# Performance work log

Measured on AMD Instinct MI355X. Metric: run time of the kernel, lower is better.

Reference implementation:

```python
import jax, jax.numpy as jnp
import numpy as np

B, K, T, C = 4, 8, 2048, 64

def setup_inputs() -> dict:
    key = jax.random.key(0)
    ks = jax.random.split(key, 7)
    return {
        "x": jax.random.normal(ks[0], (B, K, T, C), dtype=jnp.float32),
        "Wq": jax.random.normal(ks[1], (C, C), dtype=jnp.float32) / np.sqrt(C),
        "bq": jax.random.normal(ks[2], (C,), dtype=jnp.float32) * 0.01,
        "Wk": jax.random.normal(ks[3], (C, C), dtype=jnp.float32) / np.sqrt(C),
        "bk": jax.random.normal(ks[4], (C,), dtype=jnp.float32) * 0.01,
        "Wv": jax.random.normal(ks[5], (C, C), dtype=jnp.float32) / np.sqrt(C),
        "bv": jax.random.normal(ks[6], (C,), dtype=jnp.float32) * 0.01,
    }

def reference(x, Wq, bq, Wk, bk, Wv, bv):
    c_dim = x.shape[-1]
    # torch nn.Linear: y = x @ W.T + b
    q = jnp.einsum('bktc,dc->bktd', x, Wq) + bq
    k = jnp.einsum('bktc,dc->bktd', x, Wk) + bk
    v = jnp.einsum('bktc,dc->bktd', x, Wv) + bv
    scores = jnp.einsum('bkic,bkjc->bkij', q, k) / jnp.sqrt(jnp.float32(c_dim))
    attn = jax.nn.softmax(scores, axis=-1)
    out = jnp.einsum('bkij,bkjc->bkic', attn, v)
    return out
```

## Files before the change

### kernel.cpp

```cpp
#include <hip/hip_runtime.h>


#define T_DIM 2048
#define NHEAD 32
#define HSTRIDE (T_DIM * 64)
#define QSCALE 0.18033688011112042f
#define SOFF  8.0f

#define SWZ(row, grp) ((row) * 64 + ((((grp) ^ ((row) & 7)) & 7) * 8))

#define RAW_BARRIER() asm volatile("s_waitcnt lgkmcnt(0)\n\ts_barrier" ::: "memory")

typedef _Float16 h8 __attribute__((ext_vector_type(8)));
typedef _Float16 h4 __attribute__((ext_vector_type(4)));
typedef __fp16   g2 __attribute__((ext_vector_type(2)));
typedef float    f4 __attribute__((ext_vector_type(4)));
typedef float    fv16 __attribute__((ext_vector_type(16)));

union H4U { h4 v; g2 p[2]; };
union H8U { h8 v; h4 h[2]; g2 p[4]; };

#if defined(__has_builtin)
#if __has_builtin(__builtin_amdgcn_exp2f)
#define EXP2(x) __builtin_amdgcn_exp2f(x)
#endif
#endif
#ifndef EXP2
__device__ inline float exp2_raw(float x) {
    float r;
    asm("v_exp_f32 %0, %1" : "=v"(r) : "v"(x));
    return r;
}
#define EXP2(x) exp2_raw(x)
#endif

__device__ inline h4 cvt4(f4 x) {
    H4U u;
    u.p[0] = __builtin_amdgcn_cvt_pkrtz(x[0], x[1]);
    u.p[1] = __builtin_amdgcn_cvt_pkrtz(x[2], x[3]);
    return u.v;
}

__device__ inline h8 cvt8(f4 a, f4 b) {
    H8U r;
    r.h[0] = cvt4(a);
    r.h[1] = cvt4(b);
    return r.v;
}

__device__ inline fv16 splat16(float x) {
    fv16 r;
    #pragma unroll
    for (int i = 0; i < 16; ++i) r[i] = x;
    return r;
}

__global__ __launch_bounds__(256) void qkv_proj_kernel(
    const float* __restrict__ x,
    const float* __restrict__ Wq, const float* __restrict__ bq,
    const float* __restrict__ Wk, const float* __restrict__ bk,
    const float* __restrict__ Wv, const float* __restrict__ bv,
    _Float16* __restrict__ qh, _Float16* __restrict__ khT,
    _Float16* __restrict__ vtT)
{
    __shared__ _Float16 ws[3][64 * 64];
    __shared__ float bsh[3][64];

    const int tid  = threadIdx.x;
    const int row0 = blockIdx.x * 64;
    const int head = blockIdx.x >> 5;
    const int t0   = (blockIdx.x & 31) * 64;

    const int w    = tid >> 6;
    const int lane = tid & 63;
    const int l15  = lane & 15;
    const int qd   = lane >> 4;

    f4 xa[2][2];
    {
        const float* xp = x + (size_t)(row0 + w * 16 + l15) * 64 + qd * 8;
        #pragma unroll
        for (int ch = 0; ch < 2; ++ch) {
            xa[ch][0] = *(const f4*)(xp + ch * 32);
            xa[ch][1] = *(const f4*)(xp + ch * 32 + 4);
        }
    }

    #pragma unroll
    for (int m = 0; m < 3; ++m) {
        const float* Wm = (m == 0) ? Wq : ((m == 1) ? Wk : Wv);
        const float* bm = (m == 0) ? bq : ((m == 1) ? bk : bv);
        #pragma unroll
        for (int pass = 0; pass < 4; ++pass) {
            const int idx = pass * 1024 + tid * 4;
            const int d = idx >> 6, c = idx & 63;
            f4 wv = *(const f4*)(Wm + idx);
            *(h4*)&ws[m][SWZ(d, c >> 3) + (c & 7)] = cvt4(wv);
        }
        if (tid < 64) bsh[m][tid] = bm[tid];
    }

    h8 af[2];
    #pragma unroll
    for (int ch = 0; ch < 2; ++ch)
        af[ch] = cvt8(xa[ch][0], xa[ch][1]);

    __syncthreads();

    f4 acc[3][4];
    #pragma unroll
    for (int m = 0; m < 3; ++m) {
        h8 bf[4][2];
        #pragma unroll
        for (int ns = 0; ns < 4; ++ns)
            #pragma unroll
            for (int ch = 0; ch < 2; ++ch)
                bf[ns][ch] = *(const h8*)&ws[m][SWZ(ns * 16 + l15, ch * 4 + qd)];
        #pragma unroll
        for (int ns = 0; ns < 4; ++ns)
            acc[m][ns] = (f4){0.f, 0.f, 0.f, 0.f};
        #pragma unroll
        for (int ch = 0; ch < 2; ++ch)
            #pragma unroll
            for (int ns = 0; ns < 4; ++ns)
                acc[m][ns] = __builtin_amdgcn_mfma_f32_16x16x32_f16(
                    af[ch], bf[ns][ch], acc[m][ns], 0, 0, 0);
    }

    __syncthreads();

    #pragma unroll
    for (int m = 0; m < 2; ++m) {
        #pragma unroll
        for (int ns = 0; ns < 4; ++ns) {
            const int d = ns * 16 + l15;
            const float bias = bsh[m][d];
            #pragma unroll
            for (int r = 0; r < 4; ++r) {
                const int t = w * 16 + qd * 4 + r;
                float v = acc[m][ns][r] + bias;
                if (m == 0) v *= QSCALE;
                ws[m][SWZ(t, d >> 3) + (d & 7)] = (_Float16)v;
            }
        }
    }
    #pragma unroll
    for (int ns = 0; ns < 4; ++ns) {
        const int d = ns * 16 + l15;
        const float bias = bsh[2][d];
        const int tl = w * 16 + qd * 4;
        f4 pvf;
        #pragma unroll
        for (int r = 0; r < 4; ++r)
            pvf[r] = acc[2][ns][r] + bias;
        *(h4*)&ws[2][SWZ(d, tl >> 3) + (tl & 7)] = cvt4(pvf);
    }

    __syncthreads();

    #pragma unroll
    for (int pass = 0; pass < 2; ++pass) {
        const int t  = pass * 32 + (tid >> 3);
        const int c0 = (tid & 7) * 8;
        *(h8*)&qh[(size_t)(row0 + t) * 64 + c0] =
            *(const h8*)&ws[0][SWZ(t, tid & 7)];
    }
    #pragma unroll
    for (int pass = 0; pass < 2; ++pass) {
        const int f   = pass * 2048 + tid * 8;
        const int kb  = f >> 11;
        const int cs  = (f >> 9) & 3;
        const int l   = (f >> 3) & 63;
        const int p   = l & 31;
        const int w16 = p & 15;
        const int sw  = ((w16 & 12) == 4) ? (w16 + 4)
                      : (((w16 & 12) == 8) ? (w16 - 4) : w16);
        const int tact = kb * 32 + (p & 16) + sw;
        const int g8   = cs * 2 + (l >> 5);
        *(h8*)&khT[(size_t)head * HSTRIDE + (t0 >> 6) * 4096 + f] =
            *(const h8*)&ws[1][SWZ(tact, g8)];
    }
    #pragma unroll
    for (int pass = 0; pass < 2; ++pass) {
        const int f  = pass * 2048 + tid * 8;
        const int q2 = f >> 9;
        const int b  = q2 >> 1, cc = q2 & 1;
        const int l  = (f >> 3) & 63;
        const int c  = cc * 32 + (l & 31);
        const int tg = b * 2 + (l >> 5);
        *(h8*)&vtT[(size_t)head * HSTRIDE + (t0 >> 6) * 4096 + f] =
            *(const h8*)&ws[2][SWZ(c, tg)];
    }
}

__global__ __launch_bounds__(256, 2) void attn_kernel(
    const _Float16* __restrict__ qh, const _Float16* __restrict__ khT,
    const _Float16* __restrict__ vtT, float* __restrict__ out)
{
    __shared__ _Float16 tiles[3][8192];
    const int tid  = threadIdx.x;
    const int w    = tid >> 6;
    const int lane = tid & 63;

    const int bid  = blockIdx.x;
    const int xcd  = bid & 7;
    const int slot = bid >> 3;
    const int head = xcd * 4 + (slot >> 4);
    const int qpart = slot & 15;

    if (w < 2) {
        const int q0  = qpart * 128 + w * 64;
        const int l31 = lane & 31;
        const int lh  = lane >> 5;

        h8 qf[2][4];
        #pragma unroll
        for (int qs = 0; qs < 2; ++qs) {
            const _Float16* qp = qh + (size_t)(head * T_DIM + q0 + qs * 32 + l31) * 64 + lh * 8;
            #pragma unroll
            for (int cs = 0; cs < 4; ++cs)
                qf[qs][cs] = *(const h8*)(qp + cs * 16);
        }

        f4 rs4[2] = {(f4){0.f,0.f,0.f,0.f}, (f4){0.f,0.f,0.f,0.f}};
        fv16 oacc[2][2];
        #pragma unroll
        for (int qs = 0; qs < 2; ++qs)
            #pragma unroll
            for (int cc = 0; cc < 2; ++cc)
                oacc[qs][cc] = splat16(0.f);

        const int ko = lane * 8;
        const _Float16* c0 = &tiles[0][0];
        const _Float16* c1 = &tiles[1][0];
        const _Float16* c2 = &tiles[2][0];

        __syncthreads();

        fv16 st[2][2];
        #pragma unroll
        for (int kb = 0; kb < 2; ++kb) {
            h8 kf[4];
            #pragma unroll
            for (int cs = 0; cs < 4; ++cs)
                kf[cs] = *(const h8*)(c0 + kb * 2048 + cs * 512 + ko);
            st[kb][0] = splat16(-SOFF);
            st[kb][1] = splat16(-SOFF);
            #pragma unroll
            for (int cs = 0; cs < 4; ++cs)
                #pragma unroll
                for (int qs = 0; qs < 2; ++qs)
                    st[kb][qs] = __builtin_amdgcn_mfma_f32_32x32x16_f16(
                        kf[cs], qf[qs][cs], st[kb][qs], 0, 0, 0);
        }

        for (int it = 0; it < 32; ++it) {
            h8 vf[4][2];
            #pragma unroll
            for (int b = 0; b < 4; ++b)
                #pragma unroll
                for (int cc = 0; cc < 2; ++cc)
                    vf[b][cc] = *(const h8*)(c0 + 4096 + (b * 2 + cc) * 512 + ko);

            __builtin_amdgcn_s_setprio(1);

            #pragma unroll
            for (int qs = 0; qs < 2; ++qs)
                #pragma unroll
                for (int kb = 0; kb < 2; ++kb) {
                    H8U pa[2];
                    #pragma unroll
                    for (int g = 0; g < 4; ++g) {
                        f4 p;
                        p[0] = EXP2(st[kb][qs][4 * g + 0]);
                        p[1] = EXP2(st[kb][qs][4 * g + 1]);
                        p[2] = EXP2(st[kb][qs][4 * g + 2]);
                        p[3] = EXP2(st[kb][qs][4 * g + 3]);
                        rs4[qs] += p;
                        pa[g >> 1].p[(g & 1) * 2 + 0] = __builtin_amdgcn_cvt_pkrtz(p[0], p[1]);
                        pa[g >> 1].p[(g & 1) * 2 + 1] = __builtin_amdgcn_cvt_pkrtz(p[2], p[3]);
                    }
                    #pragma unroll
                    for (int bl = 0; bl < 2; ++bl) {
                        const int b = kb * 2 + bl;
                        #pragma unroll
                        for (int cc = 0; cc < 2; ++cc)
                            oacc[qs][cc] = __builtin_amdgcn_mfma_f32_32x32x16_f16(
                                pa[bl].v, vf[b][cc], oacc[qs][cc], 0, 0, 0);
                    }
                }

            if (it < 31) {
                #pragma unroll
                for (int kb = 0; kb < 2; ++kb) {
                    h8 kf[4];
                    #pragma unroll
                    for (int cs = 0; cs < 4; ++cs)
                        kf[cs] = *(const h8*)(c1 + kb * 2048 + cs * 512 + ko);
                    st[kb][0] = splat16(-SOFF);
                    st[kb][1] = splat16(-SOFF);
                    #pragma unroll
                    for (int cs = 0; cs < 4; ++cs)
                        #pragma unroll
                        for (int qs = 0; qs < 2; ++qs)
                            st[kb][qs] = __builtin_amdgcn_mfma_f32_32x32x16_f16(
                                kf[cs], qf[qs][cs], st[kb][qs], 0, 0, 0);
                }
            }

            __builtin_amdgcn_s_setprio(0);

            const _Float16* tmp = c0; c0 = c1; c1 = c2; c2 = tmp;
            __syncthreads();
        }

        #pragma unroll
        for (int qs = 0; qs < 2; ++qs) {
            float lsum = (rs4[qs][0] + rs4[qs][1]) + (rs4[qs][2] + rs4[qs][3]);
            lsum += __shfl_xor(lsum, 32, 64);
            const float linv = 1.f / lsum;
            #pragma unroll
            for (int r = 0; r < 16; ++r) {
                const int qrow = (r & 3) + 8 * (r >> 2) + 4 * lh;
                const float fac = __shfl(linv, qrow, 64);
                #pragma unroll
                for (int cc = 0; cc < 2; ++cc)
                    out[(size_t)(head * T_DIM + q0 + qs * 32 + qrow) * 64 + cc * 32 + l31] =
                        oacc[qs][cc][r] * fac;
            }
        }
    } else {
        const _Float16* src = ((w == 2) ? khT : vtT) + (size_t)head * HSTRIDE;
        const int off = (w - 2) * 4096;
        _Float16* d0 = &tiles[0][off];
        _Float16* d1 = &tiles[1][off];
        _Float16* d2 = &tiles[2][off];
        const int lo = lane * 8;
        h8 sA[8], sB[8];

        #pragma unroll
        for (int b = 0; b < 8; ++b) sA[b] = *(const h8*)(src + b * 512 + lo);
        #pragma unroll
        for (int b = 0; b < 8; ++b) sB[b] = *(const h8*)(src + 4096 + b * 512 + lo);
        #pragma unroll
        for (int b = 0; b < 8; ++b) *(h8*)(d0 + b * 512 + lo) = sA[b];
        #pragma unroll
        for (int b = 0; b < 8; ++b) *(h8*)(d1 + b * 512 + lo) = sB[b];
        #pragma unroll
        for (int b = 0; b < 8; ++b) sA[b] = *(const h8*)(src + 8192 + b * 512 + lo);
        const _Float16* sp = src + 3 * 4096;
        RAW_BARRIER();

        _Float16* w0 = d2;
        _Float16* w1 = d0;
        _Float16* w2 = d1;

        for (int t2 = 0; t2 < 16; ++t2) {
            if (t2 < 15) {
                #pragma unroll
                for (int b = 0; b < 8; ++b) sB[b] = *(const h8*)(sp + b * 512 + lo);
                sp += 4096;
                #pragma unroll
                for (int b = 0; b < 8; ++b) *(h8*)(w0 + b * 512 + lo) = sA[b];
            }
            RAW_BARRIER();
            { _Float16* t = w0; w0 = w1; w1 = w2; w2 = t; }
            if (t2 < 14) {
                #pragma unroll
                for (int b = 0; b < 8; ++b) sA[b] = *(const h8*)(sp + b * 512 + lo);
                sp += 4096;
            }
            if (t2 < 15) {
                #pragma unroll
                for (int b = 0; b < 8; ++b) *(h8*)(w0 + b * 512 + lo) = sB[b];
            }
            RAW_BARRIER();
            { _Float16* t = w0; w0 = w1; w1 = w2; w2 = t; }
        }
    }
}

extern "C" void kernel_launch(void* const* d_in, const int* in_sizes, int n_in,
                              void* d_out, int out_size, void* d_ws, size_t ws_size,
                              hipStream_t stream)
{
    (void)in_sizes; (void)n_in; (void)out_size; (void)ws_size;
    const float* x  = (const float*)d_in[0];
    const float* Wq = (const float*)d_in[1];
    const float* bq = (const float*)d_in[2];
    const float* Wk = (const float*)d_in[3];
    const float* bk = (const float*)d_in[4];
    const float* Wv = (const float*)d_in[5];
    const float* bv = (const float*)d_in[6];
    float* out = (float*)d_out;

    _Float16* qh  = (_Float16*)d_ws;
    _Float16* khT = qh + (size_t)NHEAD * HSTRIDE;
    _Float16* vtT = khT + (size_t)NHEAD * HSTRIDE;

    hipLaunchKernelGGL(qkv_proj_kernel, dim3(1024), dim3(256), 0, stream,
                       x, Wq, bq, Wk, bk, Wv, bv, qh, khT, vtT);
    hipLaunchKernelGGL(attn_kernel, dim3(512), dim3(256), 0, stream,
                       qh, khT, vtT, out);
}
```

Baseline: 136.8 us.

## Use four compute warps per block and interleave next QK^T with PV

Each block now has four compute warps covering 256 query rows instead of two warps covering 128, alongside the same two loader warps. This halves the grid and doubles how much each staged K/V tile is reused per block, reducing global-to-LDS traffic. The next-tile K loads and QK^T MFMAs are moved inside the exp/PV loop so they interleave with softmax work, and the s_setprio hints are dropped. In exchange the block gets 384 threads with the same register bound, which raises register pressure (prefetched K fragments are live throughout) and leaves fewer blocks to balance across CUs.

```diff
diff --git a/kernel.cpp b/kernel.cpp
--- a/kernel.cpp
+++ b/kernel.cpp
@@ -193,7 +193,7 @@
     }
 }
 
-__global__ __launch_bounds__(256, 2) void attn_kernel(
+__global__ __launch_bounds__(384, 2) void attn_kernel(
     const _Float16* __restrict__ qh, const _Float16* __restrict__ khT,
     const _Float16* __restrict__ vtT, float* __restrict__ out)
 {
@@ -205,11 +205,11 @@
     const int bid  = blockIdx.x;
     const int xcd  = bid & 7;
     const int slot = bid >> 3;
-    const int head = xcd * 4 + (slot >> 4);
-    const int qpart = slot & 15;
-
-    if (w < 2) {
-        const int q0  = qpart * 128 + w * 64;
+    const int head = xcd * 4 + (slot >> 3);
+    const int qpart = slot & 7;
+
+    if (w < 4) {
+        const int q0  = qpart * 256 + w * 64;
         const int l31 = lane & 31;
         const int lh  = lane >> 5;
 
@@ -255,6 +255,16 @@
         }
 
         for (int it = 0; it < 32; ++it) {
+            const bool more = (it < 31);
+
+            h8 kf[2][4];
+            if (more) {
+                #pragma unroll
+                for (int kb = 0; kb < 2; ++kb)
+                    #pragma unroll
+                    for (int cs = 0; cs < 4; ++cs)
+                        kf[kb][cs] = *(const h8*)(c1 + kb * 2048 + cs * 512 + ko);
+            }
             h8 vf[4][2];
             #pragma unroll
             for (int b = 0; b < 4; ++b)
@@ -262,23 +272,38 @@
                 for (int cc = 0; cc < 2; ++cc)
                     vf[b][cc] = *(const h8*)(c0 + 4096 + (b * 2 + cc) * 512 + ko);
 
-            __builtin_amdgcn_s_setprio(1);
-
-            #pragma unroll
-            for (int qs = 0; qs < 2; ++qs)
-                #pragma unroll
-                for (int kb = 0; kb < 2; ++kb) {
+            #pragma unroll
+            for (int kb = 0; kb < 2; ++kb)
+                #pragma unroll
+                for (int qs = 0; qs < 2; ++qs) {
+                    f4 p[2];
+                    #pragma unroll
+                    for (int g = 0; g < 4; ++g) {
+                        p[g >> 1][(g & 1) * 2 + 0] = 0.f;
+                    }
+                    f4 pg[4];
+                    #pragma unroll
+                    for (int g = 0; g < 4; ++g) {
+                        pg[g][0] = EXP2(st[kb][qs][4 * g + 0]);
+                        pg[g][1] = EXP2(st[kb][qs][4 * g + 1]);
+                        pg[g][2] = EXP2(st[kb][qs][4 * g + 2]);
+                        pg[g][3] = EXP2(st[kb][qs][4 * g + 3]);
+                        rs4[qs] += pg[g];
+                    }
+
+                    if (more) {
+                        st[kb][qs] = splat16(-SOFF);
+                        #pragma unroll
+                        for (int cs = 0; cs < 4; ++cs)
+                            st[kb][qs] = __builtin_amdgcn_mfma_f32_32x32x16_f16(
+                                kf[kb][cs], qf[qs][cs], st[kb][qs], 0, 0, 0);
+                    }
+
                     H8U pa[2];
                     #pragma unroll
                     for (int g = 0; g < 4; ++g) {
-                        f4 p;
-                        p[0] = EXP2(st[kb][qs][4 * g + 0]);
-                        p[1] = EXP2(st[kb][qs][4 * g + 1]);
-                        p[2] = EXP2(st[kb][qs][4 * g + 2]);
-                        p[3] = EXP2(st[kb][qs][4 * g + 3]);
-                        rs4[qs] += p;
-                        pa[g >> 1].p[(g & 1) * 2 + 0] = __builtin_amdgcn_cvt_pkrtz(p[0], p[1]);
-                        pa[g >> 1].p[(g & 1) * 2 + 1] = __builtin_amdgcn_cvt_pkrtz(p[2], p[3]);
+                        pa[g >> 1].p[(g & 1) * 2 + 0] = __builtin_amdgcn_cvt_pkrtz(pg[g][0], pg[g][1]);
+                        pa[g >> 1].p[(g & 1) * 2 + 1] = __builtin_amdgcn_cvt_pkrtz(pg[g][2], pg[g][3]);
                     }
                     #pragma unroll
                     for (int bl = 0; bl < 2; ++bl) {
@@ -290,26 +315,6 @@
                     }
                 }
 
-            if (it < 31) {
-                #pragma unroll
-                for (int kb = 0; kb < 2; ++kb) {
-                    h8 kf[4];
-                    #pragma unroll
-                    for (int cs = 0; cs < 4; ++cs)
-                        kf[cs] = *(const h8*)(c1 + kb * 2048 + cs * 512 + ko);
-                    st[kb][0] = splat16(-SOFF);
-                    st[kb][1] = splat16(-SOFF);
-                    #pragma unroll
-                    for (int cs = 0; cs < 4; ++cs)
-                        #pragma unroll
-                        for (int qs = 0; qs < 2; ++qs)
-                            st[kb][qs] = __builtin_amdgcn_mfma_f32_32x32x16_f16(
-                                kf[cs], qf[qs][cs], st[kb][qs], 0, 0, 0);
-                }
-            }
-
-            __builtin_amdgcn_s_setprio(0);
-
             const _Float16* tmp = c0; c0 = c1; c1 = c2; c2 = tmp;
             __syncthreads();
         }
@@ -330,8 +335,8 @@
             }
         }
     } else {
-        const _Float16* src = ((w == 2) ? khT : vtT) + (size_t)head * HSTRIDE;
-        const int off = (w - 2) * 4096;
+        const _Float16* src = ((w == 4) ? khT : vtT) + (size_t)head * HSTRIDE;
+        const int off = (w - 4) * 4096;
         _Float16* d0 = &tiles[0][off];
         _Float16* d1 = &tiles[1][off];
         _Float16* d2 = &tiles[2][off];
@@ -400,6 +405,6 @@
 
     hipLaunchKernelGGL(qkv_proj_kernel, dim3(1024), dim3(256), 0, stream,
                        x, Wq, bq, Wk, bk, Wv, bv, qh, khT, vtT);
-    hipLaunchKernelGGL(attn_kernel, dim3(512), dim3(256), 0, stream,
+    hipLaunchKernelGGL(attn_kernel, dim3(256), dim3(384), 0, stream,
                        qh, khT, vtT, out);
 }
```

Measured after the change: 135.4 us. Within noise of the previous version (-1.0%).
